# Kernel optimization log

Measured on AMD Instinct MI355X. Metric: run time of the kernel, lower is better.

## Reference

```python
import jax, jax.numpy as jnp
import numpy as np

N_GROUPS = 32
EPS = 1e-5
N_HEADS = 8
D_K = 64


def setup_inputs() -> dict:
    key = jax.random.key(0)
    ks = jax.random.split(key, 4)
    B, C, H, W = 16, 512, 32, 32
    x = jax.random.normal(ks[0], (B, C, H, W), dtype=jnp.float32)
    gn_w = jnp.ones((C,), dtype=jnp.float32)
    gn_b = jnp.zeros((C,), dtype=jnp.float32)
    proj_w = jax.random.normal(ks[1], (3 * C, C), dtype=jnp.float32) * (C ** -0.5)
    proj_b = jnp.zeros((3 * C,), dtype=jnp.float32)
    out_w = jax.random.normal(ks[2], (C, C), dtype=jnp.float32) * (C ** -0.5)
    out_b = jnp.zeros((C,), dtype=jnp.float32)
    return {"x": x, "gn_w": gn_w, "gn_b": gn_b, "proj_w": proj_w,
            "proj_b": proj_b, "out_w": out_w, "out_b": out_b}


def _group_norm(x, w, b):
    B, C, H, W = x.shape
    xg = x.reshape(B, N_GROUPS, C // N_GROUPS, H, W)
    mean = xg.mean(axis=(2, 3, 4), keepdims=True)
    var = xg.var(axis=(2, 3, 4), keepdims=True)
    xn = (xg - mean) * jax.lax.rsqrt(var + EPS)
    xn = xn.reshape(B, C, H, W)
    return xn * w[None, :, None, None] + b[None, :, None, None]


def reference(x, gn_w, gn_b, proj_w, proj_b, out_w, out_b):
    B, C, H, W = x.shape
    S = H * W
    scale = D_K ** -0.25  # applied to both q and k, as in the original
    h = _group_norm(x, gn_w, gn_b).reshape(B, C, S).transpose(0, 2, 1)  # [B,S,C]
    qkv = h @ proj_w.T + proj_b  # [B,S,3C]
    qkv = qkv.reshape(B, S, N_HEADS, 3 * D_K)
    q, k, v = jnp.split(qkv, 3, axis=-1)  # each [B,S,H,D]
    attn = jnp.einsum('bihd,bjhd->bijh', q * scale, k * scale)  # [B,S,S,Hd]
    attn = jax.nn.softmax(attn, axis=2)
    res = jnp.einsum('bijh,bjhd->bihd', attn, v).reshape(B, S, N_HEADS * D_K)
    res = res @ out_w.T + out_b  # [B,S,C]
    res = res.transpose(0, 2, 1).reshape(B, C, H, W)
    return res + x
```

## Files before the change

### kernel.cpp

```cpp
#include <hip/hip_runtime.h>
#include <stdint.h>

typedef unsigned short u16;
typedef __attribute__((ext_vector_type(8))) short bf16x8;
typedef __attribute__((ext_vector_type(4))) float f32x4;
typedef __attribute__((ext_vector_type(4))) unsigned short u16x4;

#define GLD16(gp, lp) __builtin_amdgcn_global_load_lds( \
    (__attribute__((address_space(1))) void*)(void*)(gp), \
    (__attribute__((address_space(3))) void*)(void*)(lp), 16, 0, 0)

__device__ __forceinline__ u16 f2b(float f) {
  union { float f; unsigned u; } v; v.f = f;
  unsigned r = v.u + 0x7FFFu + ((v.u >> 16) & 1u);
  return (u16)(r >> 16);
}

__global__ __launch_bounds__(256) void cvt_kernel(const float* __restrict__ w,
                                                  u16* __restrict__ o, int n4) {
  int i = blockIdx.x * 256 + threadIdx.x;
  if (i < n4) {
    const float4 f = ((const float4*)w)[i];
    u16x4 r; r[0] = f2b(f.x); r[1] = f2b(f.y); r[2] = f2b(f.z); r[3] = f2b(f.w);
    *(u16x4*)(o + (size_t)i * 4) = r;
  }
}

__global__ __launch_bounds__(256) void gn_kernel(const float* __restrict__ x,
                                                 const float* __restrict__ gw,
                                                 const float* __restrict__ gb,
                                                 u16* __restrict__ h) {
  const int b = blockIdx.x >> 5, g = blockIdx.x & 31;
  const float* xg = x + ((size_t)(b * 512 + g * 16)) * 1024;
  const int tid = threadIdx.x;
  float vals[64];
  float s = 0.f, ss = 0.f;
#pragma unroll
  for (int i = 0; i < 64; i++) {
    float vv = xg[i * 256 + tid];
    vals[i] = vv; s += vv; ss += vv * vv;
  }
#pragma unroll
  for (int off = 32; off; off >>= 1) { s += __shfl_down(s, off); ss += __shfl_down(ss, off); }
  __shared__ float red[8];
  const int wid = tid >> 6, lane = tid & 63;
  if (lane == 0) { red[wid] = s; red[4 + wid] = ss; }
  __syncthreads();
  if (tid == 0) {
    float S = red[0] + red[1] + red[2] + red[3];
    float SS = red[4] + red[5] + red[6] + red[7];
    float mean = S * (1.f / 16384.f);
    float var = SS * (1.f / 16384.f) - mean * mean;
    red[0] = mean; red[1] = rsqrtf(var + 1e-5f);
  }
  __syncthreads();
  const float mean = red[0], rs = red[1];
#pragma unroll
  for (int i = 0; i < 64; i++) {
    const int ch = i >> 2;
    const int sp = (i * 256 + tid) & 1023;
    const float sc = gw[g * 16 + ch], bi = gb[g * 16 + ch];
    const float vv = (vals[i] - mean) * rs * sc + bi;
    h[((size_t)(b * 1024 + sp)) * 512 + g * 16 + ch] = f2b(vv);
  }
}

__global__ __launch_bounds__(256) void qkv_gemm(const u16* __restrict__ h,
                                                const u16* __restrict__ w,
                                                const float* __restrict__ bias,
                                                u16* __restrict__ q,
                                                u16* __restrict__ k,
                                                u16* __restrict__ v) {
  __shared__ u16 As[128 * 32];
  __shared__ u16 Bs[128 * 32];
  const int b = blockIdx.z;
  const int bm = blockIdx.x;
  const int bn = blockIdx.y;
  const int tid = threadIdx.x, lane = tid & 63, wid = tid >> 6;
  const int wm = wid & 1, wn = wid >> 1;
  const u16* gA = h + ((size_t)b * 1024 + bm * 128) * 512;
  const u16* gB = w + (size_t)bn * 128 * 512;

  const f32x4 fz = {0.f, 0.f, 0.f, 0.f};
  f32x4 acc[4][4];
#pragma unroll
  for (int i = 0; i < 4; i++)
#pragma unroll
    for (int j = 0; j < 4; j++) acc[i][j] = fz;

  const int r0 = lane >> 2;
  const int ch8 = (lane & 3) * 8;

  for (int kt = 0; kt < 16; ++kt) {
    __syncthreads();
#pragma unroll
    for (int j = 0; j < 2; ++j) {
      const int idx = wid * 2 + j;
      const int row = idx * 16 + r0;
      GLD16(gA + (size_t)row * 512 + kt * 32 + ch8, &As[idx * 512 + lane * 8]);
      GLD16(gB + (size_t)row * 512 + kt * 32 + ch8, &Bs[idx * 512 + lane * 8]);
    }
    __syncthreads();
    bf16x8 af[4], bf[4];
#pragma unroll
    for (int mi = 0; mi < 4; mi++)
      af[mi] = *(const bf16x8*)&As[(wm * 64 + mi * 16 + (lane & 15)) * 32 + (lane >> 4) * 8];
#pragma unroll
    for (int ni = 0; ni < 4; ni++)
      bf[ni] = *(const bf16x8*)&Bs[(wn * 64 + ni * 16 + (lane & 15)) * 32 + (lane >> 4) * 8];
#pragma unroll
    for (int mi = 0; mi < 4; mi++)
#pragma unroll
      for (int ni = 0; ni < 4; ni++)
        acc[mi][ni] = __builtin_amdgcn_mfma_f32_16x16x32_bf16(af[mi], bf[ni], acc[mi][ni], 0, 0, 0);
  }

  const float scale = 0.35355339059327373f;
  const int quad4 = (lane >> 4) << 2;
#pragma unroll
  for (int mi = 0; mi < 4; mi++) {
    const int m = bm * 128 + wm * 64 + mi * 16 + quad4;
#pragma unroll
    for (int ni = 0; ni < 4; ni++) {
      const int n = bn * 128 + wn * 64 + ni * 16 + (lane & 15);
      const int head = n / 192;
      const int rr = n - head * 192;
      const float bi = bias[n];
      const int d = rr & 63;
      if (rr < 128) {
        u16* dst = (rr < 64) ? q : k;
        dst += ((size_t)(b * 8 + head) * 1024 + m) * 64 + d;
#pragma unroll
        for (int r = 0; r < 4; r++)
          dst[(size_t)r * 64] = f2b((acc[mi][ni][r] + bi) * scale);
      } else {
        u16x4 pk;
#pragma unroll
        for (int r = 0; r < 4; r++) pk[r] = f2b(acc[mi][ni][r] + bi);
        *(u16x4*)(v + ((size_t)(b * 8 + head) * 64 + d) * 1024 + m) = pk;
      }
    }
  }
}

__global__ __launch_bounds__(256) void attn_kernel(const u16* __restrict__ q,
                                                   const u16* __restrict__ k,
                                                   const u16* __restrict__ vT,
                                                   u16* __restrict__ o) {
  __shared__ u16 Ks[64 * 64];
  __shared__ u16 Vs[64 * 64];
  __shared__ u16 Ps[4][32 * 72];
  __shared__ float Li[4][32];
  const int bh = blockIdx.x;
  const int qb = blockIdx.y;
  const int tid = threadIdx.x, lane = tid & 63, wid = tid >> 6;
  const u16* Q = q + (size_t)bh * 1024 * 64;
  const u16* K = k + (size_t)bh * 1024 * 64;
  const u16* V = vT + (size_t)bh * 64 * 1024;
  const int qrow0 = qb * 128 + wid * 32;
  const int c15 = lane & 15, quad = lane >> 4;
  const int sw = c15 & 7;
  const int srow = tid >> 2;
  const int sc0 = (tid & 3) * 2;
  const int lds0 = srow * 64 + ((sc0 ^ (srow & 7)) * 8);
  const int lds1 = srow * 64 + (((sc0 + 1) ^ (srow & 7)) * 8);

  bf16x8 qf[2][2];
#pragma unroll
  for (int kk = 0; kk < 2; kk++)
#pragma unroll
    for (int ni = 0; ni < 2; ni++)
      qf[kk][ni] = *(const bf16x8*)(Q + (size_t)(qrow0 + ni * 16 + c15) * 64 + kk * 32 + quad * 8);

  const f32x4 fz = {0.f, 0.f, 0.f, 0.f};
  const float Mshift = 10.f;
  const f32x4 fm = {-Mshift, -Mshift, -Mshift, -Mshift};
  f32x4 oacc[2][4];
#pragma unroll
  for (int i = 0; i < 2; i++)
#pragma unroll
    for (int j = 0; j < 4; j++) oacc[i][j] = fz;
  float lsum[2] = {0.f, 0.f};

  u16* P = Ps[wid];

  bf16x8 kr0, kr1, vr0, vr1;
  {
    const u16* Kn = K + (size_t)srow * 64 + sc0 * 8;
    kr0 = *(const bf16x8*)(Kn); kr1 = *(const bf16x8*)(Kn + 8);
    const u16* Vn = V + (size_t)srow * 1024 + sc0 * 8;
    vr0 = *(const bf16x8*)(Vn); vr1 = *(const bf16x8*)(Vn + 8);
  }

  for (int kt = 0; kt < 16; ++kt) {
    __syncthreads();
    *(bf16x8*)&Ks[lds0] = kr0; *(bf16x8*)&Ks[lds1] = kr1;
    *(bf16x8*)&Vs[lds0] = vr0; *(bf16x8*)&Vs[lds1] = vr1;
    __syncthreads();

    {
      const int nk = (kt + 1) & 15;
      const u16* Kn = K + ((size_t)nk * 64 + srow) * 64 + sc0 * 8;
      kr0 = *(const bf16x8*)(Kn); kr1 = *(const bf16x8*)(Kn + 8);
      const u16* Vn = V + (size_t)srow * 1024 + nk * 64 + sc0 * 8;
      vr0 = *(const bf16x8*)(Vn); vr1 = *(const bf16x8*)(Vn + 8);
    }

    f32x4 sacc[4][2];
#pragma unroll
    for (int i = 0; i < 4; i++)
#pragma unroll
      for (int j = 0; j < 2; j++) sacc[i][j] = fm;
#pragma unroll
    for (int kk = 0; kk < 2; kk++) {
      bf16x8 af[4];
#pragma unroll
      for (int mi = 0; mi < 4; mi++)
        af[mi] = *(const bf16x8*)&Ks[(mi * 16 + c15) * 64 + (((kk * 4 + quad) ^ sw) * 8)];
#pragma unroll
      for (int mi = 0; mi < 4; mi++)
#pragma unroll
        for (int ni = 0; ni < 2; ni++)
          sacc[mi][ni] = __builtin_amdgcn_mfma_f32_16x16x32_bf16(af[mi], qf[kk][ni], sacc[mi][ni], 0, 0, 0);
    }

#pragma unroll
    for (int ni = 0; ni < 2; ni++) {
      const int pbase = (ni * 16 + c15) * 72;
      float ls = 0.f;
#pragma unroll
      for (int mi = 0; mi < 4; mi++) {
        unsigned pu[4];
#pragma unroll
        for (int r = 0; r < 4; r++) {
          const float p = __expf(sacc[mi][ni][r]);
          ls += p;
          union { float f; unsigned u; } c; c.f = p;
          pu[r] = c.u + 0x8000u;
        }
        uint2 pk;
        pk.x = __builtin_amdgcn_perm(pu[1], pu[0], 0x07060302u);
        pk.y = __builtin_amdgcn_perm(pu[3], pu[2], 0x07060302u);
        *(uint2*)&P[pbase + mi * 16 + quad * 4] = pk;
      }
      lsum[ni] += ls;
    }

#pragma unroll
    for (int kk = 0; kk < 2; kk++) {
      bf16x8 pf[2], vf[4];
#pragma unroll
      for (int mi = 0; mi < 2; mi++)
        pf[mi] = *(const bf16x8*)&P[(mi * 16 + c15) * 72 + kk * 32 + quad * 8];
#pragma unroll
      for (int nd = 0; nd < 4; nd++)
        vf[nd] = *(const bf16x8*)&Vs[(nd * 16 + c15) * 64 + (((kk * 4 + quad) ^ sw) * 8)];
#pragma unroll
      for (int mi = 0; mi < 2; mi++)
#pragma unroll
        for (int nd = 0; nd < 4; nd++)
          oacc[mi][nd] = __builtin_amdgcn_mfma_f32_16x16x32_bf16(pf[mi], vf[nd], oacc[mi][nd], 0, 0, 0);
    }
  }

#pragma unroll
  for (int ni = 0; ni < 2; ni++) {
    float l = lsum[ni];
    l += __shfl_xor(l, 16);
    l += __shfl_xor(l, 32);
    if (quad == 0) Li[wid][ni * 16 + c15] = 1.f / l;
  }
  const int b = bh >> 3, hh = bh & 7;
#pragma unroll
  for (int mi = 0; mi < 2; mi++) {
    const f32x4 iv = *(const f32x4*)&Li[wid][mi * 16 + quad * 4];
#pragma unroll
    for (int r = 0; r < 4; r++) {
      const int row = qrow0 + mi * 16 + quad * 4 + r;
#pragma unroll
      for (int nd = 0; nd < 4; nd++) {
        const int d = nd * 16 + c15;
        o[((size_t)b * 1024 + row) * 512 + hh * 64 + d] = f2b(oacc[mi][nd][r] * iv[r]);
      }
    }
  }
}

__global__ __launch_bounds__(256) void out_gemm(const u16* __restrict__ wo,
                                                const u16* __restrict__ attn,
                                                const float* __restrict__ ob,
                                                const float* __restrict__ x,
                                                float* __restrict__ out) {
  __shared__ u16 As[128 * 32];
  __shared__ u16 Bs[128 * 32];
  const int b = blockIdx.z;
  const int bm = blockIdx.x;
  const int bn = blockIdx.y;
  const int tid = threadIdx.x, lane = tid & 63, wid = tid >> 6;
  const int wm = wid & 1, wn = wid >> 1;
  const u16* gA = wo + (size_t)bm * 128 * 512;
  const u16* gB = attn + ((size_t)b * 1024 + bn * 128) * 512;

  const f32x4 fz = {0.f, 0.f, 0.f, 0.f};
  f32x4 acc[4][4];
#pragma unroll
  for (int i = 0; i < 4; i++)
#pragma unroll
    for (int j = 0; j < 4; j++) acc[i][j] = fz;

  const int r0 = lane >> 2;
  const int ch8 = (lane & 3) * 8;

  for (int kt = 0; kt < 16; ++kt) {
    __syncthreads();
#pragma unroll
    for (int j = 0; j < 2; ++j) {
      const int idx = wid * 2 + j;
      const int row = idx * 16 + r0;
      GLD16(gA + (size_t)row * 512 + kt * 32 + ch8, &As[idx * 512 + lane * 8]);
      GLD16(gB + (size_t)row * 512 + kt * 32 + ch8, &Bs[idx * 512 + lane * 8]);
    }
    __syncthreads();
    bf16x8 af[4], bf[4];
#pragma unroll
    for (int mi = 0; mi < 4; mi++)
      af[mi] = *(const bf16x8*)&As[(wm * 64 + mi * 16 + (lane & 15)) * 32 + (lane >> 4) * 8];
#pragma unroll
    for (int ni = 0; ni < 4; ni++)
      bf[ni] = *(const bf16x8*)&Bs[(wn * 64 + ni * 16 + (lane & 15)) * 32 + (lane >> 4) * 8];
#pragma unroll
    for (int mi = 0; mi < 4; mi++)
#pragma unroll
      for (int ni = 0; ni < 4; ni++)
        acc[mi][ni] = __builtin_amdgcn_mfma_f32_16x16x32_bf16(af[mi], bf[ni], acc[mi][ni], 0, 0, 0);
  }

  const int quad4 = (lane >> 4) << 2;
#pragma unroll
  for (int mi = 0; mi < 4; mi++) {
    const int c = bm * 128 + wm * 64 + mi * 16 + quad4;
#pragma unroll
    for (int ni = 0; ni < 4; ni++) {
      const int s = bn * 128 + wn * 64 + ni * 16 + (lane & 15);
#pragma unroll
      for (int r = 0; r < 4; r++) {
        const int cc = c + r;
        const size_t idx = ((size_t)b * 512 + cc) * 1024 + s;
        out[idx] = acc[mi][ni][r] + ob[cc] + x[idx];
      }
    }
  }
}

extern "C" void kernel_launch(void* const* d_in, const int* in_sizes, int n_in,
                              void* d_out, int out_size, void* d_ws, size_t ws_size,
                              hipStream_t stream) {
  const float* x      = (const float*)d_in[0];
  const float* gn_w   = (const float*)d_in[1];
  const float* gn_b   = (const float*)d_in[2];
  const float* proj_w = (const float*)d_in[3];
  const float* proj_b = (const float*)d_in[4];
  const float* out_w  = (const float*)d_in[5];
  const float* out_b  = (const float*)d_in[6];
  float* out = (float*)d_out;

  char* p = (char*)d_ws;
  u16* h    = (u16*)p; p += (size_t)16 * 1024 * 512 * 2;
  u16* q    = (u16*)p; p += (size_t)16 * 8 * 1024 * 64 * 2;
  u16* k    = (u16*)p; p += (size_t)16 * 8 * 1024 * 64 * 2;
  u16* v    = (u16*)p; p += (size_t)16 * 8 * 1024 * 64 * 2;
  u16* attn = (u16*)p; p += (size_t)16 * 1024 * 512 * 2;
  u16* wq   = (u16*)p; p += (size_t)1536 * 512 * 2;
  u16* wo   = (u16*)p; p += (size_t)512 * 512 * 2;

  cvt_kernel<<<768, 256, 0, stream>>>(proj_w, wq, 196608);
  cvt_kernel<<<256, 256, 0, stream>>>(out_w, wo, 65536);
  gn_kernel<<<512, 256, 0, stream>>>(x, gn_w, gn_b, h);
  qkv_gemm<<<dim3(8, 12, 16), 256, 0, stream>>>(h, wq, proj_b, q, k, v);
  attn_kernel<<<dim3(128, 8, 1), 256, 0, stream>>>(q, k, v, attn);
  out_gemm<<<dim3(4, 8, 16), 256, 0, stream>>>(wo, attn, out_b, x, out);
}
```

Before: 228.3 us.

## Load K/V fragments directly from global in attention; vectorize groupnorm stores

The attention kernel no longer stages K and V tiles through shared memory with block-wide barriers. Each wave now loads its MFMA operand fragments straight from global memory, relying on L1/L2 to serve the four waves that share a tile. This removes two __syncthreads per tile and the LDS traffic, but it quadruples global/cache load traffic and drops the register prefetch of the next tile. Separately, the groupnorm kernel now writes each spatial row's 16 channels as two 16-byte vector stores instead of 64 scattered 2-byte stores, and it folds the rsqrt into the per-channel scale.

```diff
diff --git a/kernel.cpp b/kernel.cpp
--- a/kernel.cpp
+++ b/kernel.cpp
@@ -55,13 +55,19 @@
   }
   __syncthreads();
   const float mean = red[0], rs = red[1];
-#pragma unroll
-  for (int i = 0; i < 64; i++) {
-    const int ch = i >> 2;
-    const int sp = (i * 256 + tid) & 1023;
-    const float sc = gw[g * 16 + ch], bi = gb[g * 16 + ch];
-    const float vv = (vals[i] - mean) * rs * sc + bi;
-    h[((size_t)(b * 1024 + sp)) * 512 + g * 16 + ch] = f2b(vv);
+  float sc[16], bi[16];
+#pragma unroll
+  for (int c = 0; c < 16; c++) { sc[c] = gw[g * 16 + c] * rs; bi[c] = gb[g * 16 + c]; }
+#pragma unroll
+  for (int h4 = 0; h4 < 4; h4++) {
+    const int sp = h4 * 256 + tid;
+    u16 row[16];
+#pragma unroll
+    for (int c = 0; c < 16; c++)
+      row[c] = f2b((vals[c * 4 + h4] - mean) * sc[c] + bi[c]);
+    u16* dst = h + ((size_t)(b * 1024 + sp)) * 512 + g * 16;
+    *(bf16x8*)dst = *(bf16x8*)&row[0];
+    *(bf16x8*)(dst + 8) = *(bf16x8*)&row[8];
   }
 }
 
@@ -147,8 +153,6 @@
                                                    const u16* __restrict__ k,
                                                    const u16* __restrict__ vT,
                                                    u16* __restrict__ o) {
-  __shared__ u16 Ks[64 * 64];
-  __shared__ u16 Vs[64 * 64];
   __shared__ u16 Ps[4][32 * 72];
   __shared__ float Li[4][32];
   const int bh = blockIdx.x;
@@ -159,11 +163,6 @@
   const u16* V = vT + (size_t)bh * 64 * 1024;
   const int qrow0 = qb * 128 + wid * 32;
   const int c15 = lane & 15, quad = lane >> 4;
-  const int sw = c15 & 7;
-  const int srow = tid >> 2;
-  const int sc0 = (tid & 3) * 2;
-  const int lds0 = srow * 64 + ((sc0 ^ (srow & 7)) * 8);
-  const int lds1 = srow * 64 + (((sc0 + 1) ^ (srow & 7)) * 8);
 
   bf16x8 qf[2][2];
 #pragma unroll
@@ -184,27 +183,19 @@
 
   u16* P = Ps[wid];
 
-  bf16x8 kr0, kr1, vr0, vr1;
-  {
-    const u16* Kn = K + (size_t)srow * 64 + sc0 * 8;
-    kr0 = *(const bf16x8*)(Kn); kr1 = *(const bf16x8*)(Kn + 8);
-    const u16* Vn = V + (size_t)srow * 1024 + sc0 * 8;
-    vr0 = *(const bf16x8*)(Vn); vr1 = *(const bf16x8*)(Vn + 8);
-  }
-
   for (int kt = 0; kt < 16; ++kt) {
-    __syncthreads();
-    *(bf16x8*)&Ks[lds0] = kr0; *(bf16x8*)&Ks[lds1] = kr1;
-    *(bf16x8*)&Vs[lds0] = vr0; *(bf16x8*)&Vs[lds1] = vr1;
-    __syncthreads();
-
-    {
-      const int nk = (kt + 1) & 15;
-      const u16* Kn = K + ((size_t)nk * 64 + srow) * 64 + sc0 * 8;
-      kr0 = *(const bf16x8*)(Kn); kr1 = *(const bf16x8*)(Kn + 8);
-      const u16* Vn = V + (size_t)srow * 1024 + nk * 64 + sc0 * 8;
-      vr0 = *(const bf16x8*)(Vn); vr1 = *(const bf16x8*)(Vn + 8);
-    }
+    bf16x8 af[2][4];
+#pragma unroll
+    for (int kk = 0; kk < 2; kk++)
+#pragma unroll
+      for (int mi = 0; mi < 4; mi++)
+        af[kk][mi] = *(const bf16x8*)(K + (size_t)(kt * 64 + mi * 16 + c15) * 64 + kk * 32 + quad * 8);
+    bf16x8 vf[2][4];
+#pragma unroll
+    for (int kk = 0; kk < 2; kk++)
+#pragma unroll
+      for (int nd = 0; nd < 4; nd++)
+        vf[kk][nd] = *(const bf16x8*)(V + (size_t)(nd * 16 + c15) * 1024 + kt * 64 + kk * 32 + quad * 8);
 
     f32x4 sacc[4][2];
 #pragma unroll
@@ -212,17 +203,12 @@
 #pragma unroll
       for (int j = 0; j < 2; j++) sacc[i][j] = fm;
 #pragma unroll
-    for (int kk = 0; kk < 2; kk++) {
-      bf16x8 af[4];
+    for (int kk = 0; kk < 2; kk++)
 #pragma unroll
       for (int mi = 0; mi < 4; mi++)
-        af[mi] = *(const bf16x8*)&Ks[(mi * 16 + c15) * 64 + (((kk * 4 + quad) ^ sw) * 8)];
-#pragma unroll
-      for (int mi = 0; mi < 4; mi++)
 #pragma unroll
         for (int ni = 0; ni < 2; ni++)
-          sacc[mi][ni] = __builtin_amdgcn_mfma_f32_16x16x32_bf16(af[mi], qf[kk][ni], sacc[mi][ni], 0, 0, 0);
-    }
+          sacc[mi][ni] = __builtin_amdgcn_mfma_f32_16x16x32_bf16(af[kk][mi], qf[kk][ni], sacc[mi][ni], 0, 0, 0);
 
 #pragma unroll
     for (int ni = 0; ni < 2; ni++) {
@@ -248,18 +234,15 @@
 
 #pragma unroll
     for (int kk = 0; kk < 2; kk++) {
-      bf16x8 pf[2], vf[4];
+      bf16x8 pf[2];
 #pragma unroll
       for (int mi = 0; mi < 2; mi++)
         pf[mi] = *(const bf16x8*)&P[(mi * 16 + c15) * 72 + kk * 32 + quad * 8];
 #pragma unroll
-      for (int nd = 0; nd < 4; nd++)
-        vf[nd] = *(const bf16x8*)&Vs[(nd * 16 + c15) * 64 + (((kk * 4 + quad) ^ sw) * 8)];
-#pragma unroll
       for (int mi = 0; mi < 2; mi++)
 #pragma unroll
         for (int nd = 0; nd < 4; nd++)
-          oacc[mi][nd] = __builtin_amdgcn_mfma_f32_16x16x32_bf16(pf[mi], vf[nd], oacc[mi][nd], 0, 0, 0);
+          oacc[mi][nd] = __builtin_amdgcn_mfma_f32_16x16x32_bf16(pf[mi], vf[kk][nd], oacc[mi][nd], 0, 0, 0);
     }
   }
 
```

Result: slower. 286.8 us (+25.6%).
